# Kernel optimization log

Measured on AMD Instinct MI355X. Metric: run time of the kernel, lower is better.

## Reference

```python
import jax, jax.numpy as jnp
import numpy as np

D_MODEL = 1024
H = 16
DK = D_MODEL // H


def setup_inputs() -> dict:
    key = jax.random.key(0)
    ks = jax.random.split(key, 13)
    B, S = 2, 2048
    scale = 1.0 / np.sqrt(D_MODEL)
    inp = {
        "query": jax.random.normal(ks[0], (B, S, D_MODEL), jnp.float32),
        "key": jax.random.normal(ks[1], (B, S, D_MODEL), jnp.float32),
        "value": jax.random.normal(ks[2], (B, S, D_MODEL), jnp.float32),
        "mask": jax.random.randint(ks[3], (B, 1, S, S), 0, 2, jnp.int32),
        "Wq": jax.random.normal(ks[4], (D_MODEL, D_MODEL), jnp.float32) * scale,
        "bq": jnp.zeros((D_MODEL,), jnp.float32),
        "Wk": jax.random.normal(ks[5], (D_MODEL, D_MODEL), jnp.float32) * scale,
        "bk": jnp.zeros((D_MODEL,), jnp.float32),
        "Wv": jax.random.normal(ks[6], (D_MODEL, D_MODEL), jnp.float32) * scale,
        "bv": jnp.zeros((D_MODEL,), jnp.float32),
        "Wo": jax.random.normal(ks[7], (D_MODEL, D_MODEL), jnp.float32) * scale,
        "bo": jnp.zeros((D_MODEL,), jnp.float32),
    }
    return inp


def _split_heads(x, W, b):
    # torch Linear: x @ W.T + b; then [B,S,D] -> [B,H,S,DK]
    B, S, _ = x.shape
    out = x @ W.T + b
    return out.reshape(B, S, H, DK).transpose(0, 2, 1, 3)


def reference(query, key, value, mask, Wq, bq, Wk, bk, Wv, bv, Wo, bo):
    B, S, _ = query.shape
    q = _split_heads(query, Wq, bq)   # [B,H,S,DK]
    k = _split_heads(key, Wk, bk)
    v = _split_heads(value, Wv, bv)
    scores = jnp.einsum("bhqd,bhkd->bhqk", q, k) / jnp.sqrt(jnp.asarray(DK, q.dtype))
    scores = jnp.where(mask == 0, jnp.asarray(-1e9, scores.dtype), scores)
    prob = jax.nn.softmax(scores, axis=-1)
    out = jnp.einsum("bhqk,bhkd->bhqd", prob, v)  # [B,H,S,DK]
    out = out.transpose(0, 2, 1, 3).reshape(B, S, D_MODEL)
    return out @ Wo.T + bo
```

## Files before the change

kernel.cpp:

```cpp
#include <hip/hip_runtime.h>
#include <hip/hip_bf16.h>

#define B_   2
#define S_   2048
#define DM   1024
#define NH   16
#define Mdim 4096
#define Kdim 1024

typedef __attribute__((ext_vector_type(8))) short bf16x8;
typedef __attribute__((ext_vector_type(4))) short bf16x4;
typedef __attribute__((ext_vector_type(4))) float f32x4;

__device__ __forceinline__ short f2b(float x) {
  union { __hip_bfloat16 h; short s; } u;
  u.h = __float2bfloat16(x);
  return u.s;
}

__device__ __forceinline__ size_t blk_idx(int row, int k) {
  return ((size_t)(row >> 7) * 32 + (k >> 5)) * 4096 + ((k >> 3) & 3) * 1024 +
         (row & 127) * 8 + (k & 7);
}

__device__ __forceinline__ void async_copy16(const void* g, void* l) {
  __builtin_amdgcn_global_load_lds(
      (const __attribute__((address_space(1))) unsigned int*)g,
      (__attribute__((address_space(3))) unsigned int*)l, 16, 0, 0);
}

struct Cvt7 {
  const float* src[7];
  ushort* dst[7];
  int n[7];
};

__global__ __launch_bounds__(256) void cvt_all(Cvt7 c) {
  const int ten = blockIdx.y;
  const int base = (blockIdx.x * 256 + threadIdx.x) * 8;
  if (base >= c.n[ten]) return;
  const float* s = c.src[ten] + base;
  float4 a = *(const float4*)s;
  float4 b = *(const float4*)(s + 4);
  bf16x8 r;
  r[0] = f2b(a.x); r[1] = f2b(a.y); r[2] = f2b(a.z); r[3] = f2b(a.w);
  r[4] = f2b(b.x); r[5] = f2b(b.y); r[6] = f2b(b.z); r[7] = f2b(b.w);
  const int row = base >> 10, k = base & 1023;
  *(bf16x8*)(c.dst[ten] + blk_idx(row, k)) = r;
}

__global__ __launch_bounds__(256) void pack_mask(const int* __restrict__ mask,
                                                 unsigned long long* __restrict__ mpk) {
  const int gw = (blockIdx.x * 256 + threadIdx.x) >> 6;
  const int lane = threadIdx.x & 63;
  const int mv = mask[(size_t)gw * 64 + lane];
  const unsigned long long bits = __ballot(mv != 0);
  if (lane == 0) mpk[gw] = bits;
}

template <int MODE>
__global__ __launch_bounds__(256) void gemm_pipe(const ushort* __restrict__ A,
                                                 const ushort* __restrict__ W,
                                                 const float* __restrict__ bias,
                                                 void* __restrict__ Cv, float scale) {
  const int t = threadIdx.x;
  const int w = t >> 6, lane = t & 63;
  const int quad = lane >> 4, r16 = lane & 15;
  const int wr = w >> 1, wc = w & 1;
  const int row0 = blockIdx.x * 128, col0 = blockIdx.y * 128;

  __shared__ alignas(16) ushort a_s[2][4096];
  __shared__ alignas(16) ushort b_s[2][4096];

  const ushort* Ab = A + (size_t)blockIdx.x * 32 * 4096 + (size_t)t * 8;
  const ushort* Wb = W + (size_t)blockIdx.y * 32 * 4096 + (size_t)t * 8;
  const int lo0 = w * 512, lo1 = 2048 + w * 512;

#define STAGE(buf, kb)                                   \
  do {                                                   \
    const size_t off = (size_t)(kb) * 4096;              \
    async_copy16(Ab + off, &a_s[buf][lo0]);              \
    async_copy16(Ab + off + 2048, &a_s[buf][lo1]);       \
    async_copy16(Wb + off, &b_s[buf][lo0]);              \
    async_copy16(Wb + off + 2048, &b_s[buf][lo1]);       \
  } while (0)

  f32x4 acc[4][4];
#pragma unroll
  for (int mt = 0; mt < 4; ++mt)
#pragma unroll
    for (int nt = 0; nt < 4; ++nt) acc[mt][nt] = (f32x4){0.f, 0.f, 0.f, 0.f};

  STAGE(0, 0);
  int cur = 0;
  for (int kb = 0; kb < 32; ++kb) {
    __syncthreads();
    if (kb + 1 < 32) STAGE(1 - cur, kb + 1);

    bf16x8 af[4], bfr[4];
#pragma unroll
    for (int mt = 0; mt < 4; ++mt)
      af[mt] = *(const bf16x8*)&a_s[cur][quad * 1024 + (wr * 64 + mt * 16 + r16) * 8];
#pragma unroll
    for (int nt = 0; nt < 4; ++nt)
      bfr[nt] = *(const bf16x8*)&b_s[cur][quad * 1024 + (wc * 64 + nt * 16 + r16) * 8];
#pragma unroll
    for (int mt = 0; mt < 4; ++mt)
#pragma unroll
      for (int nt = 0; nt < 4; ++nt)
        acc[mt][nt] = __builtin_amdgcn_mfma_f32_16x16x32_bf16(af[mt], bfr[nt],
                                                              acc[mt][nt], 0, 0, 0);
    cur ^= 1;
  }
#undef STAGE

#pragma unroll
  for (int mt = 0; mt < 4; ++mt) {
#pragma unroll
    for (int nt = 0; nt < 4; ++nt) {
      const int col = col0 + wc * 64 + nt * 16 + r16;
      const float bv = bias[col];
      const int rowb = row0 + wr * 64 + mt * 16 + quad * 4;
#pragma unroll
      for (int i = 0; i < 4; ++i) {
        const float v = (acc[mt][nt][i] + bv) * scale;
        const int row = rowb + i;
        if (MODE == 0) {
          ((float*)Cv)[(size_t)row * DM + col] = v;
        } else if (MODE == 1) {
          ((ushort*)Cv)[(size_t)row * DM + col] = (ushort)f2b(v);
        } else if (MODE == 2) {
          const int bb = row >> 11, s = row & (S_ - 1);
          const int hh = col >> 6, d = col & 63;
          const size_t idx = ((size_t)(bb * NH + hh) * S_ + s) * 64 +
                             (((d >> 3) ^ (s & 7)) * 8) + (d & 7);
          ((ushort*)Cv)[idx] = (ushort)f2b(v);
        } else {
          const int bb = row >> 11, s = row & (S_ - 1);
          const int hh = col >> 6, d = col & 63;
          const size_t idx = ((size_t)(bb * NH + hh) * 64 + d) * S_ + (s & ~63) +
                             ((((s >> 3) & 7) ^ (d & 7)) * 8) + (s & 7);
          ((ushort*)Cv)[idx] = (ushort)f2b(v);
        }
      }
    }
  }
}

__global__ __launch_bounds__(256) void attn_mfma(const ushort* __restrict__ Qp,
                                                 const ushort* __restrict__ Kg,
                                                 const ushort* __restrict__ Vg,
                                                 const unsigned long long* __restrict__ mpk,
                                                 ushort* __restrict__ Oa) {
  const int bh = blockIdx.y;
  const int b = bh >> 4, h = bh & 15;
  const int q0 = blockIdx.x * 64;
  const int t = threadIdx.x;
  const int w = t >> 6, lane = t & 63, quad = lane >> 4, r16 = lane & 15;
  const size_t rb = (size_t)b * S_;

  __shared__ alignas(16) ushort k_s[64 * 64];
  __shared__ alignas(16) ushort vt_s[64 * 64];
  __shared__ alignas(16) ushort p_s[4][16 * 76];

  const ushort* qptr = Qp + (rb + q0 + w * 16 + r16) * DM + h * 64 + quad * 8;
  const bf16x8 aq0 = *(const bf16x8*)qptr;
  const bf16x8 aq1 = *(const bf16x8*)(qptr + 32);

  float l_i[4] = {0.f, 0.f, 0.f, 0.f};
  f32x4 oacc[4];
#pragma unroll
  for (int nt = 0; nt < 4; ++nt) oacc[nt] = (f32x4){0.f, 0.f, 0.f, 0.f};

  const ushort* kgb = Kg + (size_t)bh * S_ * 64 + (size_t)t * 8;
  const ushort* vgb = Vg + (size_t)bh * 64 * S_ + (size_t)(t >> 3) * S_ + (t & 7) * 8;
  ushort* kl0 = &k_s[w * 512];
  ushort* kl1 = &k_s[2048 + w * 512];
  ushort* vl0 = &vt_s[w * 512];
  ushort* vl1 = &vt_s[2048 + w * 512];

  const unsigned long long* mrowp = mpk + (rb + q0 + w * 16 + quad * 4) * 32;

  for (int kt = 0; kt < S_; kt += 64) {
    __syncthreads();
    async_copy16(kgb + (size_t)kt * 64, kl0);
    async_copy16(kgb + (size_t)(kt + 32) * 64, kl1);
    async_copy16(vgb + kt, vl0);
    async_copy16(vgb + (size_t)32 * S_ + kt, vl1);
    __syncthreads();

    f32x4 sacc[4];
#pragma unroll
    for (int nt = 0; nt < 4; ++nt) {
      sacc[nt] = (f32x4){0.f, 0.f, 0.f, 0.f};
      const int krow = nt * 16 + r16;
      const bf16x8 b0 = *(const bf16x8*)&k_s[krow * 64 + ((quad ^ (krow & 7)) * 8)];
      const bf16x8 b1 = *(const bf16x8*)&k_s[krow * 64 + (((4 + quad) ^ (krow & 7)) * 8)];
      sacc[nt] = __builtin_amdgcn_mfma_f32_16x16x32_bf16(aq0, b0, sacc[nt], 0, 0, 0);
      sacc[nt] = __builtin_amdgcn_mfma_f32_16x16x32_bf16(aq1, b1, sacc[nt], 0, 0, 0);
    }

    const int seg = kt >> 6;
#pragma unroll
    for (int i = 0; i < 4; ++i) {
      const unsigned long long mbits = mrowp[i * 32 + seg];
      float ps = 0.f;
#pragma unroll
      for (int nt = 0; nt < 4; ++nt) {
        const unsigned int bit = (unsigned int)(mbits >> (nt * 16 + r16)) & 1u;
        const float p = bit ? __expf(sacc[nt][i]) : 0.f;
        ps += p;
        p_s[w][(quad * 4 + i) * 76 + nt * 16 + r16] = (ushort)f2b(p);
      }
      l_i[i] += ps;
    }

#pragma unroll
    for (int ks = 0; ks < 2; ++ks) {
      const bf16x4 lo = *(const bf16x4*)&p_s[w][r16 * 76 + ks * 32 + quad * 8];
      const bf16x4 hi = *(const bf16x4*)&p_s[w][r16 * 76 + ks * 32 + quad * 8 + 4];
      bf16x8 pa;
#pragma unroll
      for (int j = 0; j < 4; ++j) { pa[j] = lo[j]; pa[4 + j] = hi[j]; }
      const int kc = ks * 4 + quad;
#pragma unroll
      for (int nt = 0; nt < 4; ++nt) {
        const int dk = nt * 16 + r16;
        const bf16x8 vb = *(const bf16x8*)&vt_s[dk * 64 + ((kc ^ (dk & 7)) * 8)];
        oacc[nt] = __builtin_amdgcn_mfma_f32_16x16x32_bf16(pa, vb, oacc[nt], 0, 0, 0);
      }
    }
  }

#pragma unroll
  for (int i = 0; i < 4; ++i) {
    float l = l_i[i];
#pragma unroll
    for (int off = 1; off < 16; off <<= 1) l += __shfl_xor(l, off);
    l_i[i] = l;
  }
#pragma unroll
  for (int nt = 0; nt < 4; ++nt) {
#pragma unroll
    for (int i = 0; i < 4; ++i) {
      const int row = (int)rb + q0 + w * 16 + quad * 4 + i;
      const int col = h * 64 + nt * 16 + r16;
      Oa[blk_idx(row, col)] = (ushort)f2b(oacc[nt][i] / l_i[i]);
    }
  }
}

extern "C" void kernel_launch(void* const* d_in, const int* in_sizes, int n_in,
                              void* d_out, int out_size, void* d_ws, size_t ws_size,
                              hipStream_t stream) {
  const int* mask = (const int*)d_in[3];
  const float* bq = (const float*)d_in[5];
  const float* bk = (const float*)d_in[7];
  const float* bv = (const float*)d_in[9];
  const float* bo = (const float*)d_in[11];

  const size_t NE = (size_t)B_ * S_ * DM;
  const size_t NW = (size_t)DM * DM;

  ushort* qc = (ushort*)d_ws;
  ushort* kc = qc + NE;
  ushort* vc = kc + NE;
  ushort* Qp = vc + NE;
  ushort* Kg = Qp + NE;
  ushort* Vg = Kg + NE;
  ushort* Wqc = Vg + NE;
  ushort* Wkc = Wqc + NW;
  ushort* Wvc = Wkc + NW;
  ushort* Woc = Wvc + NW;
  unsigned long long* mpk = (unsigned long long*)kc;

  Cvt7 c;
  const int sidx[7] = {0, 1, 2, 4, 6, 8, 10};
  ushort* dsts[7] = {qc, kc, vc, Wqc, Wkc, Wvc, Woc};
  for (int i = 0; i < 7; ++i) {
    c.src[i] = (const float*)d_in[sidx[i]];
    c.dst[i] = dsts[i];
    c.n[i] = (i < 3) ? (int)NE : (int)NW;
  }
  cvt_all<<<dim3(2048, 7), 256, 0, stream>>>(c);

  dim3 gg(Mdim / 128, DM / 128);
  gemm_pipe<1><<<gg, 256, 0, stream>>>(qc, Wqc, bq, Qp, 0.125f);
  gemm_pipe<2><<<gg, 256, 0, stream>>>(kc, Wkc, bk, Kg, 1.0f);
  gemm_pipe<3><<<gg, 256, 0, stream>>>(vc, Wvc, bv, Vg, 1.0f);

  pack_mask<<<(B_ * S_ * (S_ / 64) * 64) / 256, 256, 0, stream>>>(mask, mpk);

  attn_mfma<<<dim3(S_ / 64, B_ * NH), 256, 0, stream>>>(Qp, Kg, Vg, mpk, qc);

  gemm_pipe<0><<<gg, 256, 0, stream>>>(qc, Woc, bo, (float*)d_out, 1.0f);
}
```

Before: 348.6 us.

## Batch QKV projections into one launch and split-K the output GEMM

Merges the three Q/K/V projection GEMMs into a single launch indexed by blockIdx.z, so each launch has three times as many blocks. The output projection now splits K in two, accumulating with float atomics into an output prefilled with the bias by a new kernel, to double its block count. The blocked layout is also changed so each row's 32 k-values sit contiguously, which changes the LDS read pattern. Risks are atomic traffic on the output, nondeterministic summation order, and possible LDS bank conflicts from the new layout.

```diff
diff --git a/kernel.cpp b/kernel.cpp
--- a/kernel.cpp
+++ b/kernel.cpp
@@ -19,8 +19,7 @@
 }
 
 __device__ __forceinline__ size_t blk_idx(int row, int k) {
-  return ((size_t)(row >> 7) * 32 + (k >> 5)) * 4096 + ((k >> 3) & 3) * 1024 +
-         (row & 127) * 8 + (k & 7);
+  return ((size_t)(row >> 7) * 32 + (k >> 5)) * 4096 + (row & 127) * 32 + (k & 31);
 }
 
 __device__ __forceinline__ void async_copy16(const void* g, void* l) {
@@ -58,11 +57,21 @@
   if (lane == 0) mpk[gw] = bits;
 }
 
-template <int MODE>
-__global__ __launch_bounds__(256) void gemm_pipe(const ushort* __restrict__ A,
-                                                 const ushort* __restrict__ W,
-                                                 const float* __restrict__ bias,
-                                                 void* __restrict__ Cv, float scale) {
+__global__ __launch_bounds__(256) void fill_bias(float* __restrict__ out,
+                                                 const float* __restrict__ bias) {
+  const int t = blockIdx.x * 256 + threadIdx.x;
+  ((float4*)out)[t] = *(const float4*)&bias[(t * 4) & (DM - 1)];
+}
+
+struct Proj {
+  const ushort* A[3];
+  const ushort* W[3];
+  const float* bias[3];
+  ushort* out[3];
+};
+
+__global__ __launch_bounds__(256) void gemm_qkv(Proj p) {
+  const int z = blockIdx.z;
   const int t = threadIdx.x;
   const int w = t >> 6, lane = t & 63;
   const int quad = lane >> 4, r16 = lane & 15;
@@ -72,17 +81,17 @@
   __shared__ alignas(16) ushort a_s[2][4096];
   __shared__ alignas(16) ushort b_s[2][4096];
 
-  const ushort* Ab = A + (size_t)blockIdx.x * 32 * 4096 + (size_t)t * 8;
-  const ushort* Wb = W + (size_t)blockIdx.y * 32 * 4096 + (size_t)t * 8;
+  const ushort* Ab = p.A[z] + (size_t)blockIdx.x * 32 * 4096 + (size_t)t * 8;
+  const ushort* Wb = p.W[z] + (size_t)blockIdx.y * 32 * 4096 + (size_t)t * 8;
   const int lo0 = w * 512, lo1 = 2048 + w * 512;
 
-#define STAGE(buf, kb)                                   \
-  do {                                                   \
-    const size_t off = (size_t)(kb) * 4096;              \
-    async_copy16(Ab + off, &a_s[buf][lo0]);              \
-    async_copy16(Ab + off + 2048, &a_s[buf][lo1]);       \
-    async_copy16(Wb + off, &b_s[buf][lo0]);              \
-    async_copy16(Wb + off + 2048, &b_s[buf][lo1]);       \
+#define STAGE(buf, kb)                                  \
+  do {                                                  \
+    const size_t off = (size_t)(kb) * 4096;             \
+    async_copy16(Ab + off, &a_s[buf][lo0]);             \
+    async_copy16(Ab + off + 2048, &a_s[buf][lo1]);      \
+    async_copy16(Wb + off, &b_s[buf][lo0]);             \
+    async_copy16(Wb + off + 2048, &b_s[buf][lo1]);      \
   } while (0)
 
   f32x4 acc[4][4];
@@ -96,14 +105,13 @@
   for (int kb = 0; kb < 32; ++kb) {
     __syncthreads();
     if (kb + 1 < 32) STAGE(1 - cur, kb + 1);
-
     bf16x8 af[4], bfr[4];
 #pragma unroll
     for (int mt = 0; mt < 4; ++mt)
-      af[mt] = *(const bf16x8*)&a_s[cur][quad * 1024 + (wr * 64 + mt * 16 + r16) * 8];
+      af[mt] = *(const bf16x8*)&a_s[cur][(wr * 64 + mt * 16 + r16) * 32 + quad * 8];
 #pragma unroll
     for (int nt = 0; nt < 4; ++nt)
-      bfr[nt] = *(const bf16x8*)&b_s[cur][quad * 1024 + (wc * 64 + nt * 16 + r16) * 8];
+      bfr[nt] = *(const bf16x8*)&b_s[cur][(wc * 64 + nt * 16 + r16) * 32 + quad * 8];
 #pragma unroll
     for (int mt = 0; mt < 4; ++mt)
 #pragma unroll
@@ -112,37 +120,93 @@
                                                               acc[mt][nt], 0, 0, 0);
     cur ^= 1;
   }
-#undef STAGE
-
+
+  const float scale = (z == 0) ? 0.125f : 1.0f;
+  ushort* Cv = p.out[z];
 #pragma unroll
   for (int mt = 0; mt < 4; ++mt) {
 #pragma unroll
     for (int nt = 0; nt < 4; ++nt) {
       const int col = col0 + wc * 64 + nt * 16 + r16;
-      const float bv = bias[col];
+      const float bv = p.bias[z][col];
       const int rowb = row0 + wr * 64 + mt * 16 + quad * 4;
 #pragma unroll
       for (int i = 0; i < 4; ++i) {
         const float v = (acc[mt][nt][i] + bv) * scale;
         const int row = rowb + i;
-        if (MODE == 0) {
-          ((float*)Cv)[(size_t)row * DM + col] = v;
-        } else if (MODE == 1) {
-          ((ushort*)Cv)[(size_t)row * DM + col] = (ushort)f2b(v);
-        } else if (MODE == 2) {
-          const int bb = row >> 11, s = row & (S_ - 1);
-          const int hh = col >> 6, d = col & 63;
+        const int bb = row >> 11, s = row & (S_ - 1);
+        const int hh = col >> 6, d = col & 63;
+        if (z == 0) {
+          Cv[(size_t)row * DM + col] = (ushort)f2b(v);
+        } else if (z == 1) {
           const size_t idx = ((size_t)(bb * NH + hh) * S_ + s) * 64 +
                              (((d >> 3) ^ (s & 7)) * 8) + (d & 7);
-          ((ushort*)Cv)[idx] = (ushort)f2b(v);
+          Cv[idx] = (ushort)f2b(v);
         } else {
-          const int bb = row >> 11, s = row & (S_ - 1);
-          const int hh = col >> 6, d = col & 63;
           const size_t idx = ((size_t)(bb * NH + hh) * 64 + d) * S_ + (s & ~63) +
                              ((((s >> 3) & 7) ^ (d & 7)) * 8) + (s & 7);
-          ((ushort*)Cv)[idx] = (ushort)f2b(v);
+          Cv[idx] = (ushort)f2b(v);
         }
       }
+    }
+  }
+}
+
+__global__ __launch_bounds__(256) void gemm_out(const ushort* __restrict__ A,
+                                                const ushort* __restrict__ W,
+                                                float* __restrict__ out) {
+  const int kz = blockIdx.z;
+  const int t = threadIdx.x;
+  const int w = t >> 6, lane = t & 63;
+  const int quad = lane >> 4, r16 = lane & 15;
+  const int wr = w >> 1, wc = w & 1;
+  const int row0 = blockIdx.x * 128, col0 = blockIdx.y * 128;
+
+  __shared__ alignas(16) ushort a_s[2][4096];
+  __shared__ alignas(16) ushort b_s[2][4096];
+
+  const ushort* Ab = A + (size_t)blockIdx.x * 32 * 4096 + (size_t)t * 8;
+  const ushort* Wb = W + (size_t)blockIdx.y * 32 * 4096 + (size_t)t * 8;
+  const int lo0 = w * 512, lo1 = 2048 + w * 512;
+
+  f32x4 acc[4][4];
+#pragma unroll
+  for (int mt = 0; mt < 4; ++mt)
+#pragma unroll
+    for (int nt = 0; nt < 4; ++nt) acc[mt][nt] = (f32x4){0.f, 0.f, 0.f, 0.f};
+
+  const int kb0 = kz * 16;
+  STAGE(0, kb0);
+  int cur = 0;
+  for (int kb = kb0; kb < kb0 + 16; ++kb) {
+    __syncthreads();
+    if (kb + 1 < kb0 + 16) STAGE(1 - cur, kb + 1);
+    bf16x8 af[4], bfr[4];
+#pragma unroll
+    for (int mt = 0; mt < 4; ++mt)
+      af[mt] = *(const bf16x8*)&a_s[cur][(wr * 64 + mt * 16 + r16) * 32 + quad * 8];
+#pragma unroll
+    for (int nt = 0; nt < 4; ++nt)
+      bfr[nt] = *(const bf16x8*)&b_s[cur][(wc * 64 + nt * 16 + r16) * 32 + quad * 8];
+#pragma unroll
+    for (int mt = 0; mt < 4; ++mt)
+#pragma unroll
+      for (int nt = 0; nt < 4; ++nt)
+        acc[mt][nt] = __builtin_amdgcn_mfma_f32_16x16x32_bf16(af[mt], bfr[nt],
+                                                              acc[mt][nt], 0, 0, 0);
+    cur ^= 1;
+  }
+#undef STAGE
+
+#pragma unroll
+  for (int mt = 0; mt < 4; ++mt) {
+#pragma unroll
+    for (int nt = 0; nt < 4; ++nt) {
+      const int col = col0 + wc * 64 + nt * 16 + r16;
+      const int rowb = row0 + wr * 64 + mt * 16 + quad * 4;
+#pragma unroll
+      for (int i = 0; i < 4; ++i)
+        unsafeAtomicAdd(&out[(size_t)(rowb + i) * DM + col], acc[mt][nt][i]);
     }
   }
 }
@@ -254,9 +318,6 @@
                               void* d_out, int out_size, void* d_ws, size_t ws_size,
                               hipStream_t stream) {
   const int* mask = (const int*)d_in[3];
-  const float* bq = (const float*)d_in[5];
-  const float* bk = (const float*)d_in[7];
-  const float* bv = (const float*)d_in[9];
   const float* bo = (const float*)d_in[11];
 
   const size_t NE = (size_t)B_ * S_ * DM;
@@ -284,14 +345,19 @@
   }
   cvt_all<<<dim3(2048, 7), 256, 0, stream>>>(c);
 
-  dim3 gg(Mdim / 128, DM / 128);
-  gemm_pipe<1><<<gg, 256, 0, stream>>>(qc, Wqc, bq, Qp, 0.125f);
-  gemm_pipe<2><<<gg, 256, 0, stream>>>(kc, Wkc, bk, Kg, 1.0f);
-  gemm_pipe<3><<<gg, 256, 0, stream>>>(vc, Wvc, bv, Vg, 1.0f);
+  Proj p;
+  p.A[0] = qc;  p.A[1] = kc;  p.A[2] = vc;
+  p.W[0] = Wqc; p.W[1] = Wkc; p.W[2] = Wvc;
+  p.bias[0] = (const float*)d_in[5];
+  p.bias[1] = (const float*)d_in[7];
+  p.bias[2] = (const float*)d_in[9];
+  p.out[0] = Qp; p.out[1] = Kg; p.out[2] = Vg;
+  gemm_qkv<<<dim3(Mdim / 128, DM / 128, 3), 256, 0, stream>>>(p);
 
   pack_mask<<<(B_ * S_ * (S_ / 64) * 64) / 256, 256, 0, stream>>>(mask, mpk);
 
   attn_mfma<<<dim3(S_ / 64, B_ * NH), 256, 0, stream>>>(Qp, Kg, Vg, mpk, qc);
 
-  gemm_pipe<0><<<gg, 256, 0, stream>>>(qc, Woc, bo, (float*)d_out, 1.0f);
-}
+  fill_bias<<<(int)(NE / 4 / 256), 256, 0, stream>>>((float*)d_out, bo);
+  gemm_out<<<dim3(Mdim / 128, DM / 128, 2), 256, 0, stream>>>(qc, Woc, (float*)d_out);
+}
```

New measurement: 310.0 us. 11.1% less time.
